# Kernel optimization log

Hardware: AMD Instinct MI355X
Metric: run time of the kernel (lower is better)

Reference implementation:

```python
import jax, jax.numpy as jnp
import numpy as np

WS = 8          # window_size
NH = 6          # num_heads
C = 192         # in_channels
HD = C // NH    # head_dim
N = WS * WS     # tokens per window


def _relative_position_index(ws):
    coords = np.stack(np.meshgrid(np.arange(ws), np.arange(ws), indexing='ij'), axis=-1).reshape(-1, 2)
    rel = coords[:, None, :] - coords[None, :, :] + (ws - 1)  # [N,N,2] in [0, 2ws-2]
    return (rel[..., 0] * (2 * ws - 1) + rel[..., 1]).astype(np.int32)  # [N,N]


def setup_inputs() -> dict:
    key = jax.random.key(0)
    ks = jax.random.split(key, 10)
    s = 0.02
    B, H, W = 8, 128, 128
    inp = {
        'x': jax.random.normal(ks[0], (B, C, H, W), dtype=jnp.float32),
        'qkv_w': jax.random.normal(ks[1], (3 * C, C), dtype=jnp.float32) * s,
        'qkv_b': jnp.zeros((3 * C,), dtype=jnp.float32),
        'proj_w': jax.random.normal(ks[2], (C, C), dtype=jnp.float32) * s,
        'proj_b': jnp.zeros((C,), dtype=jnp.float32),
        'mlp1_w': jax.random.normal(ks[3], (2 * C, C), dtype=jnp.float32) * s,
        'mlp1_b': jnp.zeros((2 * C,), dtype=jnp.float32),
        'mlp2_w': jax.random.normal(ks[4], (C, C), dtype=jnp.float32) * s,
        'mlp2_b': jnp.zeros((C,), dtype=jnp.float32),
        'bias_table': jax.random.normal(ks[5], ((2 * WS - 1) ** 2,), dtype=jnp.float32) * s,
        'rel_index': jnp.asarray(_relative_position_index(WS)),
    }
    return inp


def reference(x, qkv_w, qkv_b, proj_w, proj_b, mlp1_w, mlp1_b, mlp2_w, mlp2_b, bias_table, rel_index):
    B, _, H, W = x.shape
    nwh, nww = H // WS, W // WS
    # ---- window partition: [B,C,H,W] -> [B*nWin, N, C]
    xw = x.reshape(B, C, nwh, WS, nww, WS).transpose(0, 2, 4, 3, 5, 1).reshape(-1, N, C)
    # ---- qkv projection
    qkv = xw @ qkv_w.T + qkv_b  # [Bn, N, 3C]
    q, k, v = jnp.split(qkv, 3, axis=-1)
    split_heads = lambda t: t.reshape(-1, N, NH, HD).transpose(0, 2, 1, 3)  # [Bn,NH,N,HD]
    q, k, v = split_heads(q), split_heads(k), split_heads(v)
    # ---- learned relative-position bias (WindowScoreBias), broadcast over batch & heads
    bias = bias_table[rel_index]  # [N,N]
    scores = jnp.einsum('bhnd,bhmd->bhnm', q, k) * (1.0 / jnp.sqrt(jnp.float32(HD))) + bias
    attn = jax.nn.softmax(scores, axis=-1)
    out = jnp.einsum('bhnm,bhmd->bhnd', attn, v)  # [Bn,NH,N,HD]
    out = out.transpose(0, 2, 1, 3).reshape(-1, N, C)
    out = out @ proj_w.T + proj_b
    # ---- window merge back to BCHW
    out = out.reshape(B, nwh, nww, WS, WS, C).transpose(0, 5, 1, 3, 2, 4).reshape(B, C, H, W)
    x = x + out  # residual 1
    # ---- pointwise GLU MLP (1x1 convs as channel einsums)
    h = jnp.einsum('bchw,oc->bohw', x, mlp1_w) + mlp1_b[None, :, None, None]
    a, b = jnp.split(h, 2, axis=1)
    g = a * jax.nn.sigmoid(b)
    m = jnp.einsum('bchw,oc->bohw', g, mlp2_w) + mlp2_b[None, :, None, None]
    return x + m  # residual 2
```

## Files before the change

kernel.cpp:

```cpp
#include <hip/hip_runtime.h>


typedef short          s16x8 __attribute__((ext_vector_type(8)));
typedef unsigned short u16x4 __attribute__((ext_vector_type(4)));
typedef unsigned short u16x8 __attribute__((ext_vector_type(8)));
typedef float          f32x4 __attribute__((ext_vector_type(4)));

#define MFMA(A, B, C) __builtin_amdgcn_mfma_f32_16x16x32_bf16((A), (B), (C), 0, 0, 0)

__device__ __forceinline__ unsigned short f2b(float f) {
  unsigned x = __float_as_uint(f);
  x = (x + 0x7FFFu + ((x >> 16) & 1u)) >> 16;
  return (unsigned short)x;
}
__device__ __forceinline__ float b2f(unsigned short u) {
  return __uint_as_float(((unsigned)u) << 16);
}
__device__ __forceinline__ u16x4 pk4(f32x4 v) {
  u16x4 r;
  r[0] = f2b(v[0]); r[1] = f2b(v[1]); r[2] = f2b(v[2]); r[3] = f2b(v[3]);
  return r;
}

__device__ __forceinline__ int swz32(int t, int c) {
  return t * 32 + ((((c >> 3) ^ (t >> 1)) & 3) << 3) + (c & 7);
}
__device__ __forceinline__ int swzV(int d, int t) {
  return d * 64 + ((((t >> 3) ^ (d + (d >> 3))) & 7) << 3) + (t & 7);
}
__device__ __forceinline__ int xsw(int t, int c) {
  return t * 192 + (((c >> 3) ^ (t & 7)) << 3) + (c & 7);
}

#define XSTR   200
#define QSCALE 0.17677669529663687f

#define WOFF_QKV   0
#define WOFF_PROJ  110592
#define WOFF_MLP1  147456
#define WOFF_MLP2  221184
#define WOFF_BIASX_BYTES 516096
#define WOFF_XW_BYTES    532480

__global__ void prep_kernel(const float* __restrict__ qkv_w,
                            const float* __restrict__ proj_w,
                            const float* __restrict__ mlp1_w,
                            const float* __restrict__ mlp2_w,
                            const float* __restrict__ bias_table,
                            const int*   __restrict__ rel_index,
                            unsigned short* __restrict__ qkv_wb,
                            unsigned short* __restrict__ proj_wb,
                            unsigned short* __restrict__ mlp1_wb,
                            unsigned short* __restrict__ mlp2_wb,
                            float* __restrict__ biasx) {
  int j = blockIdx.x * 256 + threadIdx.x;
  if (j < 110592) {
    float v = qkv_w[j];
    if (j < 36864) v *= QSCALE;
    qkv_wb[j] = f2b(v);
  } else if (j < 147456) {
    proj_wb[j - 110592] = f2b(proj_w[j - 110592]);
  } else if (j < 221184) {
    mlp1_wb[j - 147456] = f2b(mlp1_w[j - 147456]);
  } else if (j < 258048) {
    mlp2_wb[j - 221184] = f2b(mlp2_w[j - 221184]);
  } else {
    int e = j - 258048;
    int l = e >> 6, v = e & 63;
    int tm = v >> 4, tn = (v >> 2) & 3, r = v & 3;
    int q = tn * 16 + (l & 15);
    int k = tm * 16 + (l >> 4) * 4 + r;
    biasx[e] = bias_table[rel_index[q * 64 + k]];
  }
}

#define TSTR 129
__global__ __launch_bounds__(256) void xpose_kernel(
    const float* __restrict__ x, unsigned short* __restrict__ xw) {
  __shared__ unsigned short tb[192 * TSTR];
  const int tid = threadIdx.x;
  const int s   = ((blockIdx.x & 7) << 7) | (blockIdx.x >> 3);
  const int b   = s >> 7;
  const int hr  = s & 127;
  const float* xrow = x + (size_t)b * 192 * 16384 + (size_t)hr * 128;

#pragma unroll
  for (int it = 0; it < 3; ++it) {
    int job = tid + 256 * it;
    int c = job >> 2, wseg = job & 3;
    const float* src = xrow + (size_t)c * 16384 + wseg * 32;
    unsigned short* dst = &tb[c * TSTR + wseg * 32];
#pragma unroll
    for (int q = 0; q < 8; ++q) {
      f32x4 v = *(const f32x4*)(src + q * 4);
      u16x4 p; p[0] = f2b(v[0]); p[1] = f2b(v[1]); p[2] = f2b(v[2]); p[3] = f2b(v[3]);
      *(u16x4*)&dst[q * 4] = p;
    }
  }
  __syncthreads();

  const int winb = b * 256 + (hr >> 3) * 16;
  const int i = hr & 7;
#pragma unroll
  for (int it = 0; it < 12; ++it) {
    int job = tid + 256 * it;
    int wwi = job / 192;
    int rem = job - wwi * 192;
    int t7 = rem / 24;
    int cseg = rem - t7 * 24;
    u16x8 v;
#pragma unroll
    for (int jj = 0; jj < 8; ++jj)
      v[jj] = tb[(cseg * 8 + jj) * TSTR + wwi * 8 + t7];
    unsigned short* dst = xw + (size_t)(winb + wwi) * 12288 + (i * 8 + t7) * 192 + cseg * 8;
    *(u16x8*)dst = v;
  }
}

__global__ __launch_bounds__(768, 3) void attn_kernel(
    unsigned short* __restrict__ xw,
    const unsigned short* __restrict__ qkv_wb, const float* __restrict__ qkv_b,
    const unsigned short* __restrict__ proj_wb, const float* __restrict__ proj_b,
    const float* __restrict__ biasx) {
  __shared__ __align__(16) unsigned short sm[24576 + 12 * 4096];

  const int tid  = threadIdx.x;
  const int lane = tid & 63;
  const int wv   = tid >> 6;
  const int wid  = (wv >= 6) ? 1 : 0;
  const int hd   = wv - wid * 6;
  const int l15  = lane & 15;
  const int lg   = lane >> 4;
  const int pair = ((blockIdx.x & 7) << 7) | (blockIdx.x >> 3);
  const int wins0 = pair * 2;
  const int oQ   = hd * 32;

#pragma unroll
  for (int it = 0; it < 4; ++it) {
    int job = tid + 768 * it;
    int wi = job / 1536;
    int j  = job - wi * 1536;
    int t  = j / 24;
    int c  = (j - t * 24) * 8;
    u16x8 v = *(const u16x8*)&xw[(size_t)(wins0 + wi) * 12288 + (size_t)j * 8];
    *(u16x8*)&sm[wi * 12288 + xsw(t, c)] = v;
  }
  __syncthreads();

  unsigned short* xa  = sm + wid * 12288;
  unsigned short* hb  = sm + 24576 + (wid * 6 + hd) * 4096;
  unsigned short* R0  = hb;
  unsigned short* R1  = hb + 2048;

  f32x4 accqT[2][4], acckT[2][4], accv[4][2];
#pragma unroll
  for (int m = 0; m < 2; ++m) {
    f32x4 bq4 = *(const f32x4*)&qkv_b[oQ + m * 16 + lg * 4];
    f32x4 bk4 = *(const f32x4*)&qkv_b[192 + oQ + m * 16 + lg * 4];
#pragma unroll
    for (int tn = 0; tn < 4; ++tn) {
      accqT[m][tn] = bq4 * QSCALE;
      acckT[m][tn] = bk4;
    }
  }
#pragma unroll
  for (int nt = 0; nt < 2; ++nt) {
    const float bv = qkv_b[384 + oQ + nt * 16 + l15];
#pragma unroll
    for (int mt = 0; mt < 4; ++mt) accv[mt][nt] = (f32x4){bv, bv, bv, bv};
  }
#pragma unroll
  for (int ks = 0; ks < 6; ++ks) {
    const int k0 = ks * 32 + lg * 8;
    s16x8 bf[4];
#pragma unroll
    for (int tn = 0; tn < 4; ++tn)
      bf[tn] = *(const s16x8*)&xa[xsw(tn * 16 + l15, k0)];
    s16x8 wq[2], wk[2], wvv[2];
#pragma unroll
    for (int m = 0; m < 2; ++m) {
      wq[m]  = *(const s16x8*)&qkv_wb[(size_t)(oQ + m * 16 + l15) * 192 + k0];
      wk[m]  = *(const s16x8*)&qkv_wb[(size_t)(192 + oQ + m * 16 + l15) * 192 + k0];
      wvv[m] = *(const s16x8*)&qkv_wb[(size_t)(384 + oQ + m * 16 + l15) * 192 + k0];
    }
#pragma unroll
    for (int m = 0; m < 2; ++m)
#pragma unroll
      for (int tn = 0; tn < 4; ++tn) {
        accqT[m][tn] = MFMA(wq[m], bf[tn], accqT[m][tn]);
        acckT[m][tn] = MFMA(wk[m], bf[tn], acckT[m][tn]);
      }
#pragma unroll
    for (int mt = 0; mt < 4; ++mt)
#pragma unroll
      for (int nt = 0; nt < 2; ++nt)
        accv[mt][nt] = MFMA(bf[mt], wvv[nt], accv[mt][nt]);
  }
#pragma unroll
  for (int m = 0; m < 2; ++m)
#pragma unroll
    for (int tn = 0; tn < 4; ++tn) {
      const int t = tn * 16 + l15, d0 = m * 16 + lg * 4;
      *(u16x4*)&R0[swz32(t, d0)] = pk4(accqT[m][tn]);
      *(u16x4*)&R1[swz32(t, d0)] = pk4(acckT[m][tn]);
    }
  u16x4 vreg[4][2];
#pragma unroll
  for (int mt = 0; mt < 4; ++mt)
#pragma unroll
    for (int nt = 0; nt < 2; ++nt)
      vreg[mt][nt] = pk4(accv[mt][nt]);

  const float* bxp = biasx + lane * 64;
  s16x8 kf[4], qf[4];
#pragma unroll
  for (int tm = 0; tm < 4; ++tm)
    kf[tm] = *(const s16x8*)&R1[swz32(tm * 16 + l15, lg * 8)];
#pragma unroll
  for (int tn = 0; tn < 4; ++tn)
    qf[tn] = *(const s16x8*)&R0[swz32(tn * 16 + l15, lg * 8)];
#pragma unroll
  for (int mt = 0; mt < 4; ++mt)
#pragma unroll
    for (int nt = 0; nt < 2; ++nt)
      *(u16x4*)&R1[swzV(nt * 16 + l15, mt * 16 + lg * 4)] = vreg[mt][nt];

  f32x4 sc[4][4];
#pragma unroll
  for (int tm = 0; tm < 4; ++tm)
#pragma unroll
    for (int tn = 0; tn < 4; ++tn) {
      f32x4 bfr = *(const f32x4*)&bxp[tm * 16 + tn * 4];
      sc[tm][tn] = MFMA(kf[tm], qf[tn], bfr);
    }
#pragma unroll
  for (int tn = 0; tn < 4; ++tn) {
    float mx = sc[0][tn][0];
#pragma unroll
    for (int tm = 0; tm < 4; ++tm)
#pragma unroll
      for (int r = 0; r < 4; ++r) mx = fmaxf(mx, sc[tm][tn][r]);
    mx = fmaxf(mx, __shfl_xor(mx, 16));
    mx = fmaxf(mx, __shfl_xor(mx, 32));
    float sum = 0.f;
#pragma unroll
    for (int tm = 0; tm < 4; ++tm)
#pragma unroll
      for (int r = 0; r < 4; ++r) {
        float e = __expf(sc[tm][tn][r] - mx);
        sc[tm][tn][r] = e;
        sum += e;
      }
    sum += __shfl_xor(sum, 16);
    sum += __shfl_xor(sum, 32);
    const float inv = 1.0f / sum;
#pragma unroll
    for (int tm = 0; tm < 4; ++tm)
#pragma unroll
      for (int r = 0; r < 4; ++r) sc[tm][tn][r] *= inv;
  }

  f32x4 oT[2][4];
#pragma unroll
  for (int m = 0; m < 2; ++m)
#pragma unroll
    for (int tn = 0; tn < 4; ++tn) oT[m][tn] = (f32x4){0.f, 0.f, 0.f, 0.f};
#pragma unroll
  for (int half = 0; half < 2; ++half) {
#pragma unroll
    for (int tm = 0; tm < 2; ++tm)
#pragma unroll
      for (int tn = 0; tn < 4; ++tn)
        *(u16x4*)&R0[swz32(tn * 16 + l15, tm * 16 + lg * 4)] =
            pk4(sc[half * 2 + tm][tn]);
    s16x8 bp[4], av[2];
#pragma unroll
    for (int tn = 0; tn < 4; ++tn)
      bp[tn] = *(const s16x8*)&R0[swz32(tn * 16 + l15, lg * 8)];
#pragma unroll
    for (int m = 0; m < 2; ++m)
      av[m] = *(const s16x8*)&R1[swzV(m * 16 + l15, half * 32 + lg * 8)];
#pragma unroll
    for (int m = 0; m < 2; ++m)
#pragma unroll
      for (int tn = 0; tn < 4; ++tn)
        oT[m][tn] = MFMA(av[m], bp[tn], oT[m][tn]);
  }
#pragma unroll
  for (int m = 0; m < 2; ++m)
#pragma unroll
    for (int tn = 0; tn < 4; ++tn)
      *(u16x4*)&R0[swz32(tn * 16 + l15, m * 16 + lg * 4)] = pk4(oT[m][tn]);
  __syncthreads();

  f32x4 pjT[2][4];
#pragma unroll
  for (int m = 0; m < 2; ++m) {
    f32x4 bp4 = *(const f32x4*)&proj_b[oQ + m * 16 + lg * 4];
#pragma unroll
    for (int tn = 0; tn < 4; ++tn) pjT[m][tn] = bp4;
  }
#pragma unroll
  for (int hh = 0; hh < 6; ++hh) {
    const unsigned short* aoh = sm + 24576 + (wid * 6 + hh) * 4096;
    s16x8 aa[4];
#pragma unroll
    for (int tn = 0; tn < 4; ++tn)
      aa[tn] = *(const s16x8*)&aoh[swz32(tn * 16 + l15, lg * 8)];
    s16x8 wp[2];
#pragma unroll
    for (int m = 0; m < 2; ++m)
      wp[m] = *(const s16x8*)&proj_wb[(size_t)(oQ + m * 16 + l15) * 192 + hh * 32 + lg * 8];
#pragma unroll
    for (int m = 0; m < 2; ++m)
#pragma unroll
      for (int tn = 0; tn < 4; ++tn)
        pjT[m][tn] = MFMA(wp[m], aa[tn], pjT[m][tn]);
  }
#pragma unroll
  for (int m = 0; m < 2; ++m)
#pragma unroll
    for (int tn = 0; tn < 4; ++tn) {
      const int t = tn * 16 + l15, o0 = oQ + m * 16 + lg * 4;
      const int ad = xsw(t, o0);
      u16x4 old = *(const u16x4*)&xa[ad];
      f32x4 s;
#pragma unroll
      for (int r = 0; r < 4; ++r) s[r] = pjT[m][tn][r] + b2f(old[r]);
      *(u16x4*)&xa[ad] = pk4(s);
    }
  __syncthreads();

#pragma unroll
  for (int it = 0; it < 4; ++it) {
    int job = tid + 768 * it;
    int wi = job / 1536;
    int j  = job - wi * 1536;
    int t  = j / 24;
    int c  = (j - t * 24) * 8;
    u16x8 v = *(const u16x8*)&sm[wi * 12288 + xsw(t, c)];
    *(u16x8*)&xw[(size_t)(wins0 + wi) * 12288 + (size_t)j * 8] = v;
  }
}

__global__ __launch_bounds__(256, 4) void mlp_kernel(
    const unsigned short* __restrict__ y_win,
    const unsigned short* __restrict__ w1b, const float* __restrict__ b1,
    const unsigned short* __restrict__ w2b, const float* __restrict__ b2,
    float* __restrict__ out) {
  __shared__ __align__(16) unsigned short sm2[2 * 64 * XSTR];
  unsigned short* yb = sm2;
  unsigned short* wk = sm2 + 64 * XSTR;

  const int tid  = threadIdx.x;
  const int lane = tid & 63;
  const int wv   = tid >> 6;
  const int l15  = lane & 15;
  const int lg   = lane >> 4;
  const int win  = ((blockIdx.x & 7) << 8) | (blockIdx.x >> 3);
  const int bb   = win >> 8;
  const int wh   = (win >> 4) & 15;
  const int wwi  = win & 15;

  const unsigned short* ywp = y_win + (size_t)win * 12288;
#pragma unroll
  for (int it = 0; it < 6; ++it) {
    int job = tid + 256 * it;
    int t = job / 24;
    int seg = job - t * 24;
    *(u16x8*)&yb[t * XSTR + seg * 8] = *(const u16x8*)&ywp[(size_t)job * 8];
  }
  __syncthreads();

#pragma unroll
  for (int i = 0; i < 3; ++i) {
    const int na = (3 * wv + i) * 16 + l15;
    const int nb = na + 192;
    f32x4 aacc[4], bacc[4];
    const float ba = b1[na], bbv = b1[nb];
#pragma unroll
    for (int m = 0; m < 4; ++m) {
      aacc[m] = (f32x4){ba, ba, ba, ba};
      bacc[m] = (f32x4){bbv, bbv, bbv, bbv};
    }
#pragma unroll
    for (int ks = 0; ks < 6; ++ks) {
      const int k0 = ks * 32 + lg * 8;
      s16x8 af[4];
#pragma unroll
      for (int m = 0; m < 4; ++m)
        af[m] = *(const s16x8*)&yb[(m * 16 + l15) * XSTR + k0];
      s16x8 wa = *(const s16x8*)&w1b[(size_t)na * 192 + k0];
      s16x8 wb = *(const s16x8*)&w1b[(size_t)nb * 192 + k0];
#pragma unroll
      for (int m = 0; m < 4; ++m) {
        aacc[m] = MFMA(af[m], wa, aacc[m]);
        bacc[m] = MFMA(af[m], wb, bacc[m]);
      }
    }
#pragma unroll
    for (int m = 0; m < 4; ++m)
#pragma unroll
      for (int r = 0; r < 4; ++r) {
        const float g = aacc[m][r] * (1.0f / (1.0f + __expf(-bacc[m][r])));
        wk[(m * 16 + lg * 4 + r) * XSTR + na] = f2b(g);
      }
  }
  __syncthreads();

  int ocol[3];
  f32x4 macc[4][3];
#pragma unroll
  for (int i = 0; i < 3; ++i) {
    ocol[i] = (3 * wv + i) * 16 + l15;
    const float bb2 = b2[ocol[i]];
#pragma unroll
    for (int m = 0; m < 4; ++m) macc[m][i] = (f32x4){bb2, bb2, bb2, bb2};
  }
#pragma unroll
  for (int ks = 0; ks < 6; ++ks) {
    const int k0 = ks * 32 + lg * 8;
    s16x8 gf[4];
#pragma unroll
    for (int m = 0; m < 4; ++m)
      gf[m] = *(const s16x8*)&wk[(m * 16 + l15) * XSTR + k0];
#pragma unroll
    for (int i = 0; i < 3; ++i) {
      s16x8 wf = *(const s16x8*)&w2b[(size_t)ocol[i] * 192 + k0];
#pragma unroll
      for (int m = 0; m < 4; ++m) macc[m][i] = MFMA(gf[m], wf, macc[m][i]);
    }
  }
  __syncthreads();
#pragma unroll
  for (int m = 0; m < 4; ++m)
#pragma unroll
    for (int i = 0; i < 3; ++i)
#pragma unroll
      for (int r = 0; r < 4; ++r)
        wk[(m * 16 + lg * 4 + r) * XSTR + ocol[i]] = f2b(macc[m][i][r]);
  __syncthreads();

  float* obase = out + (size_t)bb * 192 * 16384 + (size_t)(wh * 8) * 128 + wwi * 8;
#pragma unroll
  for (int it = 0; it < 6; ++it) {
    int job = tid + 256 * it;
    int i = job / 192;
    int c = job - i * 192;
    float vals[8];
#pragma unroll
    for (int j = 0; j < 8; ++j) {
      const int t = i * 8 + j;
      vals[j] = b2f(yb[t * XSTR + c]) + b2f(wk[t * XSTR + c]);
    }
    float* dst = obase + (size_t)c * 16384 + i * 128;
    f32x4 o0 = {vals[0], vals[1], vals[2], vals[3]};
    f32x4 o1 = {vals[4], vals[5], vals[6], vals[7]};
    *(f32x4*)dst = o0;
    *(f32x4*)(dst + 4) = o1;
  }
}

extern "C" void kernel_launch(void* const* d_in, const int* in_sizes, int n_in,
                              void* d_out, int out_size, void* d_ws, size_t ws_size,
                              hipStream_t stream) {
  (void)in_sizes; (void)n_in; (void)out_size; (void)ws_size;
  const float* x          = (const float*)d_in[0];
  const float* qkv_w      = (const float*)d_in[1];
  const float* qkv_b      = (const float*)d_in[2];
  const float* proj_w     = (const float*)d_in[3];
  const float* proj_b     = (const float*)d_in[4];
  const float* mlp1_w     = (const float*)d_in[5];
  const float* mlp1_b     = (const float*)d_in[6];
  const float* mlp2_w     = (const float*)d_in[7];
  const float* mlp2_b     = (const float*)d_in[8];
  const float* bias_table = (const float*)d_in[9];
  const int*   rel_index  = (const int*)d_in[10];
  float* out = (float*)d_out;

  char* ws = (char*)d_ws;
  unsigned short* qkv_wb  = (unsigned short*)ws + WOFF_QKV;
  unsigned short* proj_wb = (unsigned short*)ws + WOFF_PROJ;
  unsigned short* mlp1_wb = (unsigned short*)ws + WOFF_MLP1;
  unsigned short* mlp2_wb = (unsigned short*)ws + WOFF_MLP2;
  float*          biasx   = (float*)(ws + WOFF_BIASX_BYTES);
  unsigned short* xw      = (unsigned short*)(ws + WOFF_XW_BYTES);

  hipLaunchKernelGGL(prep_kernel, dim3(1024), dim3(256), 0, stream,
                     qkv_w, proj_w, mlp1_w, mlp2_w, bias_table, rel_index,
                     qkv_wb, proj_wb, mlp1_wb, mlp2_wb, biasx);
  hipLaunchKernelGGL(xpose_kernel, dim3(1024), dim3(256), 0, stream, x, xw);
  hipLaunchKernelGGL(attn_kernel, dim3(1024), dim3(768), 0, stream,
                     xw, qkv_wb, qkv_b, proj_wb, proj_b, biasx);
  hipLaunchKernelGGL(mlp_kernel, dim3(2048), dim3(256), 0, stream,
                     xw, mlp1_wb, mlp1_b, mlp2_wb, mlp2_b, out);
}
```

Before: 248.8 us.

## Fuse window partition transpose into attention kernel and stage bf16 bias in LDS

Removes the separate transpose kernel: the attention kernel now reads fp32 x directly in window order, converts to bf16 and scatters into a re-swizzled LDS tile. The relative-position bias is stored as bf16 in a new layout, loaded once per block into shared memory and added after the score MFMA instead of being read from global as the accumulator init. This drops a full bf16 round trip of the activations through global memory and one launch. In exchange it uses more LDS per block, does scalar 2-byte LDS scatter stores, and rounds the bias to bf16.

```diff
diff --git a/kernel.cpp b/kernel.cpp
--- a/kernel.cpp
+++ b/kernel.cpp
@@ -29,18 +29,22 @@
   return d * 64 + ((((t >> 3) ^ (d + (d >> 3))) & 7) << 3) + (t & 7);
 }
 __device__ __forceinline__ int xsw(int t, int c) {
-  return t * 192 + (((c >> 3) ^ (t & 7)) << 3) + (c & 7);
+  return t * 192 + ((((c >> 3) ^ ((t ^ (t >> 3)) & 7))) << 3) + (c & 7);
 }
 
 #define XSTR   200
 #define QSCALE 0.17677669529663687f
+
+#define L_BIAS 0
+#define L_XA   4096
+#define L_HD   28672
 
 #define WOFF_QKV   0
 #define WOFF_PROJ  110592
 #define WOFF_MLP1  147456
 #define WOFF_MLP2  221184
-#define WOFF_BIASX_BYTES 516096
-#define WOFF_XW_BYTES    532480
+#define WOFF_BIASB_BYTES 516096
+#define WOFF_YW_BYTES    532480
 
 __global__ void prep_kernel(const float* __restrict__ qkv_w,
                             const float* __restrict__ proj_w,
@@ -52,7 +56,7 @@
                             unsigned short* __restrict__ proj_wb,
                             unsigned short* __restrict__ mlp1_wb,
                             unsigned short* __restrict__ mlp2_wb,
-                            float* __restrict__ biasx) {
+                            unsigned short* __restrict__ biasb) {
   int j = blockIdx.x * 256 + threadIdx.x;
   if (j < 110592) {
     float v = qkv_w[j];
@@ -66,63 +70,21 @@
     mlp2_wb[j - 221184] = f2b(mlp2_w[j - 221184]);
   } else {
     int e = j - 258048;
-    int l = e >> 6, v = e & 63;
+    int v = e >> 6, l = e & 63;
     int tm = v >> 4, tn = (v >> 2) & 3, r = v & 3;
     int q = tn * 16 + (l & 15);
     int k = tm * 16 + (l >> 4) * 4 + r;
-    biasx[e] = bias_table[rel_index[q * 64 + k]];
-  }
-}
-
-#define TSTR 129
-__global__ __launch_bounds__(256) void xpose_kernel(
-    const float* __restrict__ x, unsigned short* __restrict__ xw) {
-  __shared__ unsigned short tb[192 * TSTR];
-  const int tid = threadIdx.x;
-  const int s   = ((blockIdx.x & 7) << 7) | (blockIdx.x >> 3);
-  const int b   = s >> 7;
-  const int hr  = s & 127;
-  const float* xrow = x + (size_t)b * 192 * 16384 + (size_t)hr * 128;
-
-#pragma unroll
-  for (int it = 0; it < 3; ++it) {
-    int job = tid + 256 * it;
-    int c = job >> 2, wseg = job & 3;
-    const float* src = xrow + (size_t)c * 16384 + wseg * 32;
-    unsigned short* dst = &tb[c * TSTR + wseg * 32];
-#pragma unroll
-    for (int q = 0; q < 8; ++q) {
-      f32x4 v = *(const f32x4*)(src + q * 4);
-      u16x4 p; p[0] = f2b(v[0]); p[1] = f2b(v[1]); p[2] = f2b(v[2]); p[3] = f2b(v[3]);
-      *(u16x4*)&dst[q * 4] = p;
-    }
-  }
-  __syncthreads();
-
-  const int winb = b * 256 + (hr >> 3) * 16;
-  const int i = hr & 7;
-#pragma unroll
-  for (int it = 0; it < 12; ++it) {
-    int job = tid + 256 * it;
-    int wwi = job / 192;
-    int rem = job - wwi * 192;
-    int t7 = rem / 24;
-    int cseg = rem - t7 * 24;
-    u16x8 v;
-#pragma unroll
-    for (int jj = 0; jj < 8; ++jj)
-      v[jj] = tb[(cseg * 8 + jj) * TSTR + wwi * 8 + t7];
-    unsigned short* dst = xw + (size_t)(winb + wwi) * 12288 + (i * 8 + t7) * 192 + cseg * 8;
-    *(u16x8*)dst = v;
+    biasb[e] = f2b(bias_table[rel_index[q * 64 + k]]);
   }
 }
 
 __global__ __launch_bounds__(768, 3) void attn_kernel(
-    unsigned short* __restrict__ xw,
+    const float* __restrict__ x,
     const unsigned short* __restrict__ qkv_wb, const float* __restrict__ qkv_b,
     const unsigned short* __restrict__ proj_wb, const float* __restrict__ proj_b,
-    const float* __restrict__ biasx) {
-  __shared__ __align__(16) unsigned short sm[24576 + 12 * 4096];
+    const unsigned short* __restrict__ biasb,
+    unsigned short* __restrict__ yw) {
+  __shared__ __align__(16) unsigned short sm[77824];
 
   const int tid  = threadIdx.x;
   const int lane = tid & 63;
@@ -135,20 +97,35 @@
   const int wins0 = pair * 2;
   const int oQ   = hd * 32;
 
+  if (tid < 512)
+    *(u16x8*)&sm[L_BIAS + tid * 8] = *(const u16x8*)&biasb[tid * 8];
+
+  const float* xwb[2];
+#pragma unroll
+  for (int wi = 0; wi < 2; ++wi) {
+    const int w = wins0 + wi;
+    xwb[wi] = x + (size_t)(w >> 8) * 192 * 16384
+                + (size_t)(((w >> 4) & 15) * 8) * 128 + (w & 15) * 8;
+  }
 #pragma unroll
   for (int it = 0; it < 4; ++it) {
     int job = tid + 768 * it;
     int wi = job / 1536;
     int j  = job - wi * 1536;
-    int t  = j / 24;
-    int c  = (j - t * 24) * 8;
-    u16x8 v = *(const u16x8*)&xw[(size_t)(wins0 + wi) * 12288 + (size_t)j * 8];
-    *(u16x8*)&sm[wi * 12288 + xsw(t, c)] = v;
-  }
-  __syncthreads();
-
-  unsigned short* xa  = sm + wid * 12288;
-  unsigned short* hb  = sm + 24576 + (wid * 6 + hd) * 4096;
+    int c = j >> 3, i = j & 7;
+    const float* src = xwb[wi] + (size_t)c * 16384 + i * 128;
+    f32x4 v0 = *(const f32x4*)(src);
+    f32x4 v1 = *(const f32x4*)(src + 4);
+    unsigned short* xa_ = sm + L_XA + wi * 12288;
+#pragma unroll
+    for (int r = 0; r < 4; ++r) xa_[xsw(i * 8 + r, c)] = f2b(v0[r]);
+#pragma unroll
+    for (int r = 0; r < 4; ++r) xa_[xsw(i * 8 + 4 + r, c)] = f2b(v1[r]);
+  }
+  __syncthreads();
+
+  unsigned short* xa  = sm + L_XA + wid * 12288;
+  unsigned short* hb  = sm + L_HD + (wid * 6 + hd) * 4096;
   unsigned short* R0  = hb;
   unsigned short* R1  = hb + 2048;
 
@@ -211,7 +188,6 @@
     for (int nt = 0; nt < 2; ++nt)
       vreg[mt][nt] = pk4(accv[mt][nt]);
 
-  const float* bxp = biasx + lane * 64;
   s16x8 kf[4], qf[4];
 #pragma unroll
   for (int tm = 0; tm < 4; ++tm)
@@ -225,14 +201,20 @@
     for (int nt = 0; nt < 2; ++nt)
       *(u16x4*)&R1[swzV(nt * 16 + l15, mt * 16 + lg * 4)] = vreg[mt][nt];
 
+  const f32x4 z4 = {0.f, 0.f, 0.f, 0.f};
   f32x4 sc[4][4];
 #pragma unroll
   for (int tm = 0; tm < 4; ++tm)
 #pragma unroll
-    for (int tn = 0; tn < 4; ++tn) {
-      f32x4 bfr = *(const f32x4*)&bxp[tm * 16 + tn * 4];
-      sc[tm][tn] = MFMA(kf[tm], qf[tn], bfr);
-    }
+    for (int tn = 0; tn < 4; ++tn)
+      sc[tm][tn] = MFMA(kf[tm], qf[tn], z4);
+#pragma unroll
+  for (int tm = 0; tm < 4; ++tm)
+#pragma unroll
+    for (int tn = 0; tn < 4; ++tn)
+#pragma unroll
+      for (int r = 0; r < 4; ++r)
+        sc[tm][tn][r] += b2f(sm[L_BIAS + ((tm * 16 + tn * 4 + r) << 6) + lane]);
 #pragma unroll
   for (int tn = 0; tn < 4; ++tn) {
     float mx = sc[0][tn][0];
@@ -264,7 +246,7 @@
 #pragma unroll
   for (int m = 0; m < 2; ++m)
 #pragma unroll
-    for (int tn = 0; tn < 4; ++tn) oT[m][tn] = (f32x4){0.f, 0.f, 0.f, 0.f};
+    for (int tn = 0; tn < 4; ++tn) oT[m][tn] = z4;
 #pragma unroll
   for (int half = 0; half < 2; ++half) {
 #pragma unroll
@@ -302,7 +284,7 @@
   }
 #pragma unroll
   for (int hh = 0; hh < 6; ++hh) {
-    const unsigned short* aoh = sm + 24576 + (wid * 6 + hh) * 4096;
+    const unsigned short* aoh = sm + L_HD + (wid * 6 + hh) * 4096;
     s16x8 aa[4];
 #pragma unroll
     for (int tn = 0; tn < 4; ++tn)
@@ -338,8 +320,8 @@
     int j  = job - wi * 1536;
     int t  = j / 24;
     int c  = (j - t * 24) * 8;
-    u16x8 v = *(const u16x8*)&sm[wi * 12288 + xsw(t, c)];
-    *(u16x8*)&xw[(size_t)(wins0 + wi) * 12288 + (size_t)j * 8] = v;
+    u16x8 v = *(const u16x8*)&sm[L_XA + wi * 12288 + xsw(t, c)];
+    *(u16x8*)&yw[(size_t)(wins0 + wi) * 12288 + (size_t)j * 8] = v;
   }
 }
 
@@ -483,15 +465,14 @@
   unsigned short* proj_wb = (unsigned short*)ws + WOFF_PROJ;
   unsigned short* mlp1_wb = (unsigned short*)ws + WOFF_MLP1;
   unsigned short* mlp2_wb = (unsigned short*)ws + WOFF_MLP2;
-  float*          biasx   = (float*)(ws + WOFF_BIASX_BYTES);
-  unsigned short* xw      = (unsigned short*)(ws + WOFF_XW_BYTES);
+  unsigned short* biasb   = (unsigned short*)(ws + WOFF_BIASB_BYTES);
+  unsigned short* yw      = (unsigned short*)(ws + WOFF_YW_BYTES);
 
   hipLaunchKernelGGL(prep_kernel, dim3(1024), dim3(256), 0, stream,
                      qkv_w, proj_w, mlp1_w, mlp2_w, bias_table, rel_index,
-                     qkv_wb, proj_wb, mlp1_wb, mlp2_wb, biasx);
-  hipLaunchKernelGGL(xpose_kernel, dim3(1024), dim3(256), 0, stream, x, xw);
+                     qkv_wb, proj_wb, mlp1_wb, mlp2_wb, biasb);
   hipLaunchKernelGGL(attn_kernel, dim3(1024), dim3(768), 0, stream,
-                     xw, qkv_wb, qkv_b, proj_wb, proj_b, biasx);
+                     x, qkv_wb, qkv_b, proj_wb, proj_b, biasb, yw);
   hipLaunchKernelGGL(mlp_kernel, dim3(2048), dim3(256), 0, stream,
-                     xw, mlp1_wb, mlp1_b, mlp2_wb, mlp2_b, out);
-}
+                     yw, mlp1_wb, mlp1_b, mlp2_wb, mlp2_b, out);
+}
```

Measured after the change: 241.6 us. -2.9%, faster.
